# Performance work log

Hardware: AMD Instinct MI355X
Metric: run time of the kernel (lower is better)

Reference implementation:

```python
import jax, jax.numpy as jnp
import numpy as np

DIST_THRESH = 0.1
W_DIST = 0.05
W_CHAMFER = 0.05
W_SEP = 0.0005


def setup_inputs() -> dict:
    key = jax.random.key(0)
    k1, k2, k3, k4 = jax.random.split(key, 4)
    B, N, K = 4, 200000, 64
    return {
        "landmarks_C": jax.random.uniform(k1, (B, N, 3), jnp.float32),          # predicted point coords
        "landmarks_F": jax.random.normal(k2, (B, N, 4), jnp.float32) * 0.05,    # [dist, dx, dy, dz]
        "targets_C": jax.random.uniform(k3, (B, K, 3), jnp.float32),            # GT landmark coords
        "targets_F": jax.random.randint(k4, (B, K), 0, 8),                      # GT landmark class labels
        "classes": jnp.arange(6),                                               # classes to supervise
    }


def reference(landmarks_C, landmarks_F, targets_C, targets_F, classes):
    def per_batch(C_i, F_i, tC, tF):
        # class mask over GT landmarks (replaces boolean indexing in torch)
        mask_k = jnp.any(tF[None, :] == classes[:, None], axis=0)          # [K]
        n_valid = mask_k.sum()
        dists_i = F_i[:, 0]                                                # predicted distance, [N]
        coords_i = C_i + F_i[:, 1:]                                        # refined coords, [N,3]
        # pairwise dists GT landmarks -> raw point coords, invalid classes pushed to +inf
        pd = jnp.linalg.norm(C_i[None, :, :] - tC[:, None, :], axis=-1)    # [K,N]
        pd = jnp.where(mask_k[:, None], pd, jnp.inf)
        min_d = pd.min(axis=0)                                             # [N]
        pm = min_d < DIST_THRESH                                           # points near some GT landmark
        # smooth-L1 (beta=1, sum) on predicted distance; clip(inf)=2*thresh reproduces empty-target fallback
        tgt = jnp.clip(min_d, 0.0, 2.0 * DIST_THRESH)
        diff = dists_i - tgt
        ad = jnp.abs(diff)
        dist_loss = jnp.where(ad < 1.0, 0.5 * diff * diff, ad - 0.5).sum()
        # pairwise dists GT landmarks -> refined coords
        ld = jnp.linalg.norm(coords_i[None, :, :] - tC[:, None, :], axis=-1)  # [K,N]
        ld_m = jnp.where(mask_k[:, None], ld, jnp.inf)
        p2g = jnp.where(pm, ld_m.min(axis=0), 0.0)                         # pred->gt, masked points only
        g2p = jnp.where(mask_k, ld_m.min(axis=1), 0.0)                     # gt->pred, valid GT only
        chamfer = (p2g * p2g).sum() + (g2p * g2p).sum()
        # separation: ratio of dists to 2 nearest (valid) GT landmarks, per masked point
        _, idx = jax.lax.top_k(-pd.T, 2)                                   # [N,2] indices of 2 smallest
        d01 = jnp.take_along_axis(ld.T, idx, axis=1)                       # [N,2]
        sep = jnp.where(pm, d01[:, 0] / d01[:, 1], 0.0).sum()
        sep = jnp.where(n_valid >= 2, sep, 0.0)
        return W_DIST * dist_loss + W_CHAMFER * chamfer + W_SEP * sep

    losses = jax.vmap(per_batch)(landmarks_C, landmarks_F, targets_C, targets_F)
    return losses.mean()
```

## Files before the change

kernel.cpp:

```cpp
#include <hip/hip_runtime.h>


constexpr int KT = 64;
constexpr int P  = 8;
constexpr int NREP = 16;
constexpr float DIST_THRESH = 0.1f;
constexpr float W_DIST    = 0.05f;
constexpr float W_CHAMFER = 0.05f;
constexpr float W_SEP     = 0.0005f;
constexpr float PT_SENT = -1e18f;
constexpr float TG_SENT = -1e18f;
constexpr float BIGF  = 3.0e38f;
constexpr float WBIAS = 16.0f;

typedef float f2 __attribute__((ext_vector_type(2)));

__device__ __forceinline__ unsigned umin_(unsigned a, unsigned b) { return a < b ? a : b; }
__device__ __forceinline__ unsigned umax_(unsigned a, unsigned b) { return a > b ? a : b; }

__device__ __forceinline__ f2 pk_fma(f2 a, f2 b, f2 c) {
#if __has_builtin(__builtin_elementwise_fma)
    return __builtin_elementwise_fma(a, b, c);
#else
    f2 r; r.x = fmaf(a.x, b.x, c.x); r.y = fmaf(a.y, b.y, c.y); return r;
#endif
}

__global__ __launch_bounds__(128, 3)
void landmark_main(const float* __restrict__ C, const float* __restrict__ F,
                   const float* __restrict__ tC, const int* __restrict__ tF,
                   const int* __restrict__ classes, int n_classes,
                   int N, unsigned int* __restrict__ g2p_rep,
                   float* __restrict__ sums_rep)
{
    __shared__ float4 tgtH2[2][64];
    __shared__ float4 tgtFull[KT];
    __shared__ unsigned g2pLDS[KT];
    __shared__ unsigned mK1[64][P];
    __shared__ unsigned mK2[64][P];
    __shared__ float    mLM[64][P];

    const int tid   = threadIdx.x;
    const int lane  = tid & 63;
    const int h     = tid >> 6;
    const int l31   = lane & 31;
    const int blk   = blockIdx.x;
    const int b     = blk & 3;
    const int chunk = blk >> 2;
    const int rep   = chunk & (NREP - 1);
    const unsigned kbase = (unsigned)(h << 5);

    if (tid < KT) {
        int f = tF[b * KT + tid];
        bool valid = false;
        for (int c = 0; c < n_classes; ++c) valid = valid || (f == classes[c]);
        float x = TG_SENT, y = TG_SENT, z = TG_SENT;
        if (valid) {
            x = tC[(b * KT + tid) * 3 + 0];
            y = tC[(b * KT + tid) * 3 + 1];
            z = tC[(b * KT + tid) * 3 + 2];
        }
        float4 v = make_float4(-2.f * x, -2.f * y, -2.f * z,
                               x * x + y * y + z * z + WBIAS);
        tgtFull[tid] = v;
        int hh = tid >> 5, j = tid & 31;
        tgtH2[hh][j] = v;
        tgtH2[hh][j + 32] = v;
        g2pLDS[tid] = 0x7F7FFFFFu;
    }
    __syncthreads();

    const float*  Cb = C + (size_t)b * N * 3;
    const float4* Fb = (const float4*)(F + (size_t)b * N * 4);
    const int base = chunk * (64 * P);

    f2 pcx[P], pcy[P], pcz[P];
    float ccm[P], f0[P];
    #pragma unroll
    for (int p = 0; p < P; ++p) {
        int n = base + p * 64 + lane;
        bool v = (n < N);
        int ni = v ? n : 0;
        float4 f4 = Fb[ni];
        float X = Cb[3 * ni + 0], Y = Cb[3 * ni + 1], Z = Cb[3 * ni + 2];
        f0[p] = v ? f4.x : 2.0f * DIST_THRESH;
        if (!v) { X = PT_SENT; Y = PT_SENT; Z = PT_SENT; f4.y = f4.z = f4.w = 0.f; }
        float cxv = X + f4.y, cyv = Y + f4.z, czv = Z + f4.w;
        pcx[p] = (f2){X, cxv};
        pcy[p] = (f2){Y, cyv};
        pcz[p] = (f2){Z, czv};
        ccm[p] = fmaf(czv, czv, fmaf(cyv, cyv, cxv * cxv)) - WBIAS;
    }

    unsigned k1[P], k2[P];
    float lmin[P];
    #pragma unroll
    for (int p = 0; p < P; ++p) { k1[p] = 0xFFFFFFFFu; k2[p] = 0xFFFFFFFFu; lmin[p] = BIGF; }

    const float4* TH = tgtH2[h];

    #pragma unroll 4
    for (int i = 0; i < 32; ++i) {
        const float4 T = TH[l31 + i];
        const unsigned tk = kbase | (unsigned)((l31 + i) & 31);
        const f2 Tx = {T.x, T.x}, Ty = {T.y, T.y}, Tz = {T.z, T.z}, Tw = {T.w, T.w};
        float av[P];
        #pragma unroll
        for (int p = 0; p < P; ++p) {
            f2 w = pk_fma(pcx[p], Tx, pk_fma(pcy[p], Ty, pk_fma(pcz[p], Tz, Tw)));
            unsigned key = (__float_as_uint(w.x) & 0xFFFFFFC0u) | tk;
            unsigned hi = umax_(k1[p], key);
            k1[p] = umin_(k1[p], key);
            k2[p] = umin_(k2[p], hi);
            lmin[p] = fminf(lmin[p], w.y);
            av[p] = w.y + ccm[p];
        }
        float dl = fminf(fminf(fminf(av[0], av[1]), fminf(av[2], av[3])),
                         fminf(fminf(av[4], av[5]), fminf(av[6], av[7])));
        dl = fmaxf(dl, 0.f);
        atomicMin(&g2pLDS[tk], __float_as_uint(dl));
    }

    if (h == 0) {
        #pragma unroll
        for (int p = 0; p < P; ++p) {
            mK1[lane][p] = k1[p];
            mK2[lane][p] = k2[p];
            mLM[lane][p] = lmin[p];
        }
    }
    __syncthreads();

    if (h == 0) {
        atomicMax(&g2p_rep[rep * 256 + b * 64 + lane], ~g2pLDS[lane]);
    } else {
        float dist_acc = 0.f, p2g_acc = 0.f, sep_acc = 0.f;
        #pragma unroll
        for (int p = 0; p < P; ++p) {
            unsigned a1 = mK1[lane][p], a2 = mK2[lane][p];
            float    al = mLM[lane][p];
            unsigned m1 = umin_(a1, k1[p]);
            unsigned m2 = umin_(umax_(a1, k1[p]), umin_(a2, k2[p]));
            float lm = fminf(al, lmin[p]);
            float X = pcx[p].x, Y = pcy[p].x, Z = pcz[p].x;
            float ppm = fmaf(Z, Z, fmaf(Y, Y, X * X)) - WBIAS;
            float keyf1 = __uint_as_float(m1 & 0xFFFFFFC0u);
            float mind = sqrtf(fmaxf(keyf1 + ppm, 0.f));
            bool pm = mind < DIST_THRESH;
            float tgtv = fminf(mind, 2.0f * DIST_THRESH);
            float diff = f0[p] - tgtv;
            float ad = fabsf(diff);
            dist_acc += (ad < 1.0f) ? 0.5f * diff * diff : (ad - 0.5f);
            if (pm) {
                p2g_acc += fmaxf(lm + ccm[p], 0.f);
                int i1 = (int)(m1 & 63u), i2 = (int)(m2 & 63u);
                float4 T1 = tgtFull[i1], T2 = tgtFull[i2];
                float cxv = pcx[p].y, cyv = pcy[p].y, czv = pcz[p].y;
                float l1sq = fmaf(cxv, T1.x, fmaf(cyv, T1.y, fmaf(czv, T1.z, T1.w))) + ccm[p];
                float l2sq = fmaf(cxv, T2.x, fmaf(cyv, T2.y, fmaf(czv, T2.z, T2.w))) + ccm[p];
                sep_acc += sqrtf(fmaxf(l1sq, 0.f) / fmaxf(l2sq, 1e-30f));
            }
        }

        float v0 = dist_acc, v1 = p2g_acc, v2 = sep_acc;
        #pragma unroll
        for (int o = 32; o > 0; o >>= 1) {
            v0 += __shfl_down(v0, o, 64);
            v1 += __shfl_down(v1, o, 64);
            v2 += __shfl_down(v2, o, 64);
        }
        if (lane == 0) {
            float* sb = sums_rep + rep * 16 + b;
            atomicAdd(sb + 0, v0);
            atomicAdd(sb + 4, v1);
            atomicAdd(sb + 8, v2);
        }
    }
}

__global__ void landmark_finalize(const int* __restrict__ tF, const int* __restrict__ classes,
                                  int n_classes, const unsigned int* __restrict__ g2p_rep,
                                  const float* __restrict__ sums_rep, float* __restrict__ out)
{
    __shared__ float lossb[4];
    const int tid = threadIdx.x;
    const int b = tid >> 6, k = tid & 63;

    int f = tF[b * KT + k];
    bool valid = false;
    for (int c = 0; c < n_classes; ++c) valid = valid || (f == classes[c]);

    unsigned enc = 0;
    for (int r = 0; r < NREP; ++r) enc = umax_(enc, g2p_rep[r * 256 + b * 64 + k]);
    float g  = valid ? __uint_as_float(~enc) : 0.f;
    float nv = valid ? 1.f : 0.f;

    #pragma unroll
    for (int o = 32; o > 0; o >>= 1) {
        g  += __shfl_down(g, o, 64);
        nv += __shfl_down(nv, o, 64);
    }
    if (k == 0) {
        float sd = 0.f, sp = 0.f, ss = 0.f;
        for (int r = 0; r < NREP; ++r) {
            sd += sums_rep[r * 16 + 0 + b];
            sp += sums_rep[r * 16 + 4 + b];
            ss += sums_rep[r * 16 + 8 + b];
        }
        float sep = (nv >= 2.f) ? ss : 0.f;
        lossb[b] = W_DIST * sd + W_CHAMFER * (sp + g) + W_SEP * sep;
    }
    __syncthreads();
    if (tid == 0)
        out[0] = (lossb[0] + lossb[1] + lossb[2] + lossb[3]) * 0.25f;
}

extern "C" void kernel_launch(void* const* d_in, const int* in_sizes, int n_in,
                              void* d_out, int out_size, void* d_ws, size_t ws_size,
                              hipStream_t stream)
{
    const float* C       = (const float*)d_in[0];
    const float* F       = (const float*)d_in[1];
    const float* tC      = (const float*)d_in[2];
    const int*   tF      = (const int*)d_in[3];
    const int*   classes = (const int*)d_in[4];
    const int n_classes = in_sizes[4];
    const int B = 4;
    const int N = in_sizes[0] / (3 * B);

    unsigned int* g2p_rep  = (unsigned int*)d_ws;
    float*        sums_rep = (float*)((char*)d_ws + NREP * 256 * 4);

    hipMemsetAsync(d_ws, 0, NREP * 256 * 4 + NREP * 16 * 4, stream);

    const int cpb = (N + 64 * P - 1) / (64 * P);
    landmark_main<<<cpb * 4, 128, 0, stream>>>(C, F, tC, tF, classes, n_classes,
                                               N, g2p_rep, sums_rep);
    landmark_finalize<<<1, 256, 0, stream>>>(tF, classes, n_classes, g2p_rep,
                                             sums_rep, (float*)d_out);
}
```

Measured before the change: 103.7 us.

## Split targets across four waves, precompute targets in setup kernel, shuffle-reduce g2p

Target preprocessing (class masking, packed -2x/|x|^2 form) moves into a separate one-block setup kernel that writes to workspace. The main kernel now uses 256-thread blocks with 4 points per lane instead of 8, and each wave takes a 16-target slice. Each wave reads its targets as uniform (scalar) global loads instead of the rotated LDS copy. The per-target gt->pred minimum is reduced with cross-lane xor shuffles and one lane's global atomics, replacing per-iteration LDS atomicMin. Per-point top-2 keys from three waves are merged through LDS by the fourth wave. The aim is more parallelism and less LDS traffic, at the cost of an extra kernel launch and a sizeable shuffle reduction.

Result: slower. 172.0 us (+65.9%).

```diff
diff --git a/kernel.cpp b/kernel.cpp
--- a/kernel.cpp
+++ b/kernel.cpp
@@ -2,7 +2,7 @@
 
 
 constexpr int KT = 64;
-constexpr int P  = 8;
+constexpr int P  = 4;
 constexpr int NREP = 16;
 constexpr float DIST_THRESH = 0.1f;
 constexpr float W_DIST    = 0.05f;
@@ -26,49 +26,46 @@
 #endif
 }
 
-__global__ __launch_bounds__(128, 3)
+
+__global__ void landmark_setup(const float* __restrict__ tC, const int* __restrict__ tF,
+                               const int* __restrict__ classes, int n_classes,
+                               float4* __restrict__ tws)
+{
+    const int t = threadIdx.x;
+    const int b = t >> 6, k = t & 63;
+    int f = tF[b * KT + k];
+    bool valid = false;
+    for (int c = 0; c < n_classes; ++c) valid = valid || (f == classes[c]);
+    float x = TG_SENT, y = TG_SENT, z = TG_SENT;
+    if (valid) {
+        x = tC[(b * KT + k) * 3 + 0];
+        y = tC[(b * KT + k) * 3 + 1];
+        z = tC[(b * KT + k) * 3 + 2];
+    }
+    tws[b * KT + k] = make_float4(-2.f * x, -2.f * y, -2.f * z,
+                                  x * x + y * y + z * z + WBIAS);
+}
+
+__global__ __launch_bounds__(256, 4)
 void landmark_main(const float* __restrict__ C, const float* __restrict__ F,
-                   const float* __restrict__ tC, const int* __restrict__ tF,
-                   const int* __restrict__ classes, int n_classes,
-                   int N, unsigned int* __restrict__ g2p_rep,
-                   float* __restrict__ sums_rep)
-{
-    __shared__ float4 tgtH2[2][64];
-    __shared__ float4 tgtFull[KT];
-    __shared__ unsigned g2pLDS[KT];
-    __shared__ unsigned mK1[64][P];
-    __shared__ unsigned mK2[64][P];
-    __shared__ float    mLM[64][P];
+                   const float4* __restrict__ tws, int N,
+                   unsigned int* __restrict__ g2p_rep, float* __restrict__ sums_rep)
+{
+    __shared__ float4 tgtLDS[KT];
+    __shared__ uint4  pubK1[3][64];
+    __shared__ uint4  pubK2[3][64];
+    __shared__ float4 pubLM[3][64];
 
     const int tid   = threadIdx.x;
     const int lane  = tid & 63;
-    const int h     = tid >> 6;
-    const int l31   = lane & 31;
+    const int wib   = tid >> 6;
+    const int ksplit = __builtin_amdgcn_readfirstlane(wib);
     const int blk   = blockIdx.x;
     const int b     = blk & 3;
     const int chunk = blk >> 2;
     const int rep   = chunk & (NREP - 1);
-    const unsigned kbase = (unsigned)(h << 5);
-
-    if (tid < KT) {
-        int f = tF[b * KT + tid];
-        bool valid = false;
-        for (int c = 0; c < n_classes; ++c) valid = valid || (f == classes[c]);
-        float x = TG_SENT, y = TG_SENT, z = TG_SENT;
-        if (valid) {
-            x = tC[(b * KT + tid) * 3 + 0];
-            y = tC[(b * KT + tid) * 3 + 1];
-            z = tC[(b * KT + tid) * 3 + 2];
-        }
-        float4 v = make_float4(-2.f * x, -2.f * y, -2.f * z,
-                               x * x + y * y + z * z + WBIAS);
-        tgtFull[tid] = v;
-        int hh = tid >> 5, j = tid & 31;
-        tgtH2[hh][j] = v;
-        tgtH2[hh][j + 32] = v;
-        g2pLDS[tid] = 0x7F7FFFFFu;
-    }
-    __syncthreads();
+
+    if (wib == 0) tgtLDS[lane] = tws[b * KT + lane];
 
     const float*  Cb = C + (size_t)b * N * 3;
     const float4* Fb = (const float4*)(F + (size_t)b * N * 4);
@@ -93,16 +90,16 @@
     }
 
     unsigned k1[P], k2[P];
-    float lmin[P];
+    float lmin[P], dlreg[16];
     #pragma unroll
     for (int p = 0; p < P; ++p) { k1[p] = 0xFFFFFFFFu; k2[p] = 0xFFFFFFFFu; lmin[p] = BIGF; }
 
-    const float4* TH = tgtH2[h];
-
-    #pragma unroll 4
-    for (int i = 0; i < 32; ++i) {
-        const float4 T = TH[l31 + i];
-        const unsigned tk = kbase | (unsigned)((l31 + i) & 31);
+    const float4* tb = tws + b * KT + ksplit * 16;
+
+    #pragma unroll
+    for (int i = 0; i < 16; ++i) {
+        const float4 T = tb[i];
+        const unsigned tk = (unsigned)(ksplit * 16 + i);
         const f2 Tx = {T.x, T.x}, Ty = {T.y, T.y}, Tz = {T.z, T.z}, Tw = {T.w, T.w};
         float av[P];
         #pragma unroll
@@ -115,33 +112,49 @@
             lmin[p] = fminf(lmin[p], w.y);
             av[p] = w.y + ccm[p];
         }
-        float dl = fminf(fminf(fminf(av[0], av[1]), fminf(av[2], av[3])),
-                         fminf(fminf(av[4], av[5]), fminf(av[6], av[7])));
-        dl = fmaxf(dl, 0.f);
-        atomicMin(&g2pLDS[tk], __float_as_uint(dl));
-    }
-
-    if (h == 0) {
+        dlreg[i] = fmaxf(fminf(fminf(av[0], av[1]), fminf(av[2], av[3])), 0.f);
+    }
+
+    #pragma unroll
+    for (int d = 1; d < 64; d <<= 1) {
+        #pragma unroll
+        for (int i = 0; i < 16; ++i)
+            dlreg[i] = fminf(dlreg[i], __shfl_xor(dlreg[i], d, 64));
+    }
+    if (lane == 0) {
+        unsigned gb = rep * 256 + b * 64 + ksplit * 16;
+        #pragma unroll
+        for (int i = 0; i < 16; ++i)
+            atomicMax(&g2p_rep[gb + i], ~__float_as_uint(dlreg[i]));
+    }
+
+    if (wib < 3) {
+        pubK1[wib][lane] = make_uint4(k1[0], k1[1], k1[2], k1[3]);
+        pubK2[wib][lane] = make_uint4(k2[0], k2[1], k2[2], k2[3]);
+        pubLM[wib][lane] = make_float4(lmin[0], lmin[1], lmin[2], lmin[3]);
+    }
+    __syncthreads();
+
+    if (wib == 3) {
+        float dist_acc = 0.f, p2g_acc = 0.f, sep_acc = 0.f;
+        uint4 K1s[3], K2s[3]; float4 LMs[3];
+        #pragma unroll
+        for (int w = 0; w < 3; ++w) {
+            K1s[w] = pubK1[w][lane]; K2s[w] = pubK2[w][lane]; LMs[w] = pubLM[w][lane];
+        }
         #pragma unroll
         for (int p = 0; p < P; ++p) {
-            mK1[lane][p] = k1[p];
-            mK2[lane][p] = k2[p];
-            mLM[lane][p] = lmin[p];
-        }
-    }
-    __syncthreads();
-
-    if (h == 0) {
-        atomicMax(&g2p_rep[rep * 256 + b * 64 + lane], ~g2pLDS[lane]);
-    } else {
-        float dist_acc = 0.f, p2g_acc = 0.f, sep_acc = 0.f;
-        #pragma unroll
-        for (int p = 0; p < P; ++p) {
-            unsigned a1 = mK1[lane][p], a2 = mK2[lane][p];
-            float    al = mLM[lane][p];
-            unsigned m1 = umin_(a1, k1[p]);
-            unsigned m2 = umin_(umax_(a1, k1[p]), umin_(a2, k2[p]));
-            float lm = fminf(al, lmin[p]);
+            unsigned m1 = k1[p], m2 = k2[p];
+            float lm = lmin[p];
+            #pragma unroll
+            for (int w = 0; w < 3; ++w) {
+                unsigned o1 = (p == 0) ? K1s[w].x : (p == 1) ? K1s[w].y : (p == 2) ? K1s[w].z : K1s[w].w;
+                unsigned o2 = (p == 0) ? K2s[w].x : (p == 1) ? K2s[w].y : (p == 2) ? K2s[w].z : K2s[w].w;
+                float    ol = (p == 0) ? LMs[w].x : (p == 1) ? LMs[w].y : (p == 2) ? LMs[w].z : LMs[w].w;
+                m2 = umin_(umax_(m1, o1), umin_(m2, o2));
+                m1 = umin_(m1, o1);
+                lm = fminf(lm, ol);
+            }
             float X = pcx[p].x, Y = pcy[p].x, Z = pcz[p].x;
             float ppm = fmaf(Z, Z, fmaf(Y, Y, X * X)) - WBIAS;
             float keyf1 = __uint_as_float(m1 & 0xFFFFFFC0u);
@@ -154,7 +167,7 @@
             if (pm) {
                 p2g_acc += fmaxf(lm + ccm[p], 0.f);
                 int i1 = (int)(m1 & 63u), i2 = (int)(m2 & 63u);
-                float4 T1 = tgtFull[i1], T2 = tgtFull[i2];
+                float4 T1 = tgtLDS[i1], T2 = tgtLDS[i2];
                 float cxv = pcx[p].y, cyv = pcy[p].y, czv = pcz[p].y;
                 float l1sq = fmaf(cxv, T1.x, fmaf(cyv, T1.y, fmaf(czv, T1.z, T1.w))) + ccm[p];
                 float l2sq = fmaf(cxv, T2.x, fmaf(cyv, T2.y, fmaf(czv, T2.z, T2.w))) + ccm[p];
@@ -230,12 +243,14 @@
 
     unsigned int* g2p_rep  = (unsigned int*)d_ws;
     float*        sums_rep = (float*)((char*)d_ws + NREP * 256 * 4);
+    float4*       tws      = (float4*)((char*)d_ws + NREP * 256 * 4 + NREP * 16 * 4);
 
     hipMemsetAsync(d_ws, 0, NREP * 256 * 4 + NREP * 16 * 4, stream);
 
+    landmark_setup<<<1, 256, 0, stream>>>(tC, tF, classes, n_classes, tws);
+
     const int cpb = (N + 64 * P - 1) / (64 * P);
-    landmark_main<<<cpb * 4, 128, 0, stream>>>(C, F, tC, tF, classes, n_classes,
-                                               N, g2p_rep, sums_rep);
+    landmark_main<<<cpb * 4, 256, 0, stream>>>(C, F, tws, N, g2p_rep, sums_rep);
     landmark_finalize<<<1, 256, 0, stream>>>(tF, classes, n_classes, g2p_rep,
                                              sums_rep, (float*)d_out);
 }
```

## Split target halves within a wave and merge top-2 via cross-half shuffles

Applied to the files above, without the earlier changes.

Each wave now handles its own chunk of points: the two 32-lane halves each scan 32 targets over 4 points per lane (an XOR-indexed target walk instead of a duplicated target table), and the per-point top-2 keys and min values are merged with a lane-xor-32 shuffle instead of a shared-memory exchange between two waves. Blocks grow to 256 threads holding four independent waves, with one block-level reduction of the partial sums before the global atomics. The aim is to drop the block-wide sync and LDS round trip of the old two-wave split and to lower per-thread register load for better occupancy. In exchange there are more shuffles, fewer points per thread to amortize each target fetch, and a 4-way reduction step.

After: 105.4 us. Within noise of the previous version (+1.7%).

```diff
diff --git a/kernel.cpp b/kernel.cpp
--- a/kernel.cpp
+++ b/kernel.cpp
@@ -2,7 +2,7 @@
 
 
 constexpr int KT = 64;
-constexpr int P  = 8;
+constexpr int P  = 4;
 constexpr int NREP = 16;
 constexpr float DIST_THRESH = 0.1f;
 constexpr float W_DIST    = 0.05f;
@@ -26,29 +26,26 @@
 #endif
 }
 
-__global__ __launch_bounds__(128, 3)
+__global__ __launch_bounds__(256, 6)
 void landmark_main(const float* __restrict__ C, const float* __restrict__ F,
                    const float* __restrict__ tC, const int* __restrict__ tF,
                    const int* __restrict__ classes, int n_classes,
-                   int N, unsigned int* __restrict__ g2p_rep,
-                   float* __restrict__ sums_rep)
+                   int N, int cpb,
+                   unsigned int* __restrict__ g2p_rep, float* __restrict__ sums_rep)
 {
-    __shared__ float4 tgtH2[2][64];
-    __shared__ float4 tgtFull[KT];
+    __shared__ float4 tgt[KT];
     __shared__ unsigned g2pLDS[KT];
-    __shared__ unsigned mK1[64][P];
-    __shared__ unsigned mK2[64][P];
-    __shared__ float    mLM[64][P];
+    __shared__ float rs[3][4];
 
     const int tid   = threadIdx.x;
     const int lane  = tid & 63;
-    const int h     = tid >> 6;
+    const int wib   = tid >> 6;
     const int l31   = lane & 31;
+    const int half  = lane >> 5;
     const int blk   = blockIdx.x;
     const int b     = blk & 3;
-    const int chunk = blk >> 2;
-    const int rep   = chunk & (NREP - 1);
-    const unsigned kbase = (unsigned)(h << 5);
+    const int chunk = (blk >> 2) * 4 + wib;
+    const int rep   = blk & (NREP - 1);
 
     if (tid < KT) {
         int f = tF[b * KT + tid];
@@ -60,91 +57,78 @@
             y = tC[(b * KT + tid) * 3 + 1];
             z = tC[(b * KT + tid) * 3 + 2];
         }
-        float4 v = make_float4(-2.f * x, -2.f * y, -2.f * z,
+        tgt[tid] = make_float4(-2.f * x, -2.f * y, -2.f * z,
                                x * x + y * y + z * z + WBIAS);
-        tgtFull[tid] = v;
-        int hh = tid >> 5, j = tid & 31;
-        tgtH2[hh][j] = v;
-        tgtH2[hh][j + 32] = v;
         g2pLDS[tid] = 0x7F7FFFFFu;
     }
     __syncthreads();
 
-    const float*  Cb = C + (size_t)b * N * 3;
-    const float4* Fb = (const float4*)(F + (size_t)b * N * 4);
-    const int base = chunk * (64 * P);
-
-    f2 pcx[P], pcy[P], pcz[P];
-    float ccm[P], f0[P];
-    #pragma unroll
-    for (int p = 0; p < P; ++p) {
-        int n = base + p * 64 + lane;
-        bool v = (n < N);
-        int ni = v ? n : 0;
-        float4 f4 = Fb[ni];
-        float X = Cb[3 * ni + 0], Y = Cb[3 * ni + 1], Z = Cb[3 * ni + 2];
-        f0[p] = v ? f4.x : 2.0f * DIST_THRESH;
-        if (!v) { X = PT_SENT; Y = PT_SENT; Z = PT_SENT; f4.y = f4.z = f4.w = 0.f; }
-        float cxv = X + f4.y, cyv = Y + f4.z, czv = Z + f4.w;
-        pcx[p] = (f2){X, cxv};
-        pcy[p] = (f2){Y, cyv};
-        pcz[p] = (f2){Z, czv};
-        ccm[p] = fmaf(czv, czv, fmaf(cyv, cyv, cxv * cxv)) - WBIAS;
-    }
-
-    unsigned k1[P], k2[P];
-    float lmin[P];
-    #pragma unroll
-    for (int p = 0; p < P; ++p) { k1[p] = 0xFFFFFFFFu; k2[p] = 0xFFFFFFFFu; lmin[p] = BIGF; }
-
-    const float4* TH = tgtH2[h];
-
-    #pragma unroll 4
-    for (int i = 0; i < 32; ++i) {
-        const float4 T = TH[l31 + i];
-        const unsigned tk = kbase | (unsigned)((l31 + i) & 31);
-        const f2 Tx = {T.x, T.x}, Ty = {T.y, T.y}, Tz = {T.z, T.z}, Tw = {T.w, T.w};
-        float av[P];
+    float dist_acc = 0.f, p2g_acc = 0.f, sep_acc = 0.f;
+
+    if (chunk < cpb) {
+        const float*  Cb = C + (size_t)b * N * 3;
+        const float4* Fb = (const float4*)(F + (size_t)b * N * 4);
+        const int base = chunk * (32 * P);
+
+        f2 pcx[P], pcy[P], pcz[P];
+        float ccm[P], f0[P];
         #pragma unroll
         for (int p = 0; p < P; ++p) {
-            f2 w = pk_fma(pcx[p], Tx, pk_fma(pcy[p], Ty, pk_fma(pcz[p], Tz, Tw)));
-            unsigned key = (__float_as_uint(w.x) & 0xFFFFFFC0u) | tk;
-            unsigned hi = umax_(k1[p], key);
-            k1[p] = umin_(k1[p], key);
-            k2[p] = umin_(k2[p], hi);
-            lmin[p] = fminf(lmin[p], w.y);
-            av[p] = w.y + ccm[p];
-        }
-        float dl = fminf(fminf(fminf(av[0], av[1]), fminf(av[2], av[3])),
-                         fminf(fminf(av[4], av[5]), fminf(av[6], av[7])));
-        dl = fmaxf(dl, 0.f);
-        atomicMin(&g2pLDS[tk], __float_as_uint(dl));
-    }
-
-    if (h == 0) {
+            int n = base + p * 32 + l31;
+            bool v = (n < N);
+            int ni = v ? n : 0;
+            float4 f4 = Fb[ni];
+            float X = Cb[3 * ni + 0], Y = Cb[3 * ni + 1], Z = Cb[3 * ni + 2];
+            f0[p] = v ? f4.x : 2.0f * DIST_THRESH;
+            if (!v) { X = PT_SENT; Y = PT_SENT; Z = PT_SENT; f4.y = f4.z = f4.w = 0.f; }
+            float cxv = X + f4.y, cyv = Y + f4.z, czv = Z + f4.w;
+            pcx[p] = (f2){X, cxv};
+            pcy[p] = (f2){Y, cyv};
+            pcz[p] = (f2){Z, czv};
+            ccm[p] = fmaf(czv, czv, fmaf(cyv, cyv, cxv * cxv)) - WBIAS;
+        }
+
+        unsigned k1[P], k2[P];
+        float lmin[P];
+        #pragma unroll
+        for (int p = 0; p < P; ++p) { k1[p] = 0xFFFFFFFFu; k2[p] = 0xFFFFFFFFu; lmin[p] = BIGF; }
+
+        #pragma unroll 8
+        for (int i = 0; i < 32; ++i) {
+            const unsigned tk = (unsigned)(lane ^ i);
+            const float4 T = tgt[tk];
+            const f2 Tx = {T.x, T.x}, Ty = {T.y, T.y}, Tz = {T.z, T.z}, Tw = {T.w, T.w};
+            float av[P];
+            #pragma unroll
+            for (int p = 0; p < P; ++p) {
+                f2 w = pk_fma(pcx[p], Tx, pk_fma(pcy[p], Ty, pk_fma(pcz[p], Tz, Tw)));
+                unsigned key = (__float_as_uint(w.x) & 0xFFFFFFC0u) | tk;
+                unsigned hi = umax_(k1[p], key);
+                k1[p] = umin_(k1[p], key);
+                k2[p] = umin_(k2[p], hi);
+                lmin[p] = fminf(lmin[p], w.y);
+                av[p] = w.y + ccm[p];
+            }
+            float dl = fmaxf(fminf(fminf(av[0], av[1]), fminf(av[2], av[3])), 0.f);
+            atomicMin(&g2pLDS[tk], __float_as_uint(dl));
+        }
+
         #pragma unroll
         for (int p = 0; p < P; ++p) {
-            mK1[lane][p] = k1[p];
-            mK2[lane][p] = k2[p];
-            mLM[lane][p] = lmin[p];
-        }
-    }
-    __syncthreads();
-
-    if (h == 0) {
-        atomicMax(&g2p_rep[rep * 256 + b * 64 + lane], ~g2pLDS[lane]);
-    } else {
-        float dist_acc = 0.f, p2g_acc = 0.f, sep_acc = 0.f;
-        #pragma unroll
-        for (int p = 0; p < P; ++p) {
-            unsigned a1 = mK1[lane][p], a2 = mK2[lane][p];
-            float    al = mLM[lane][p];
-            unsigned m1 = umin_(a1, k1[p]);
-            unsigned m2 = umin_(umax_(a1, k1[p]), umin_(a2, k2[p]));
-            float lm = fminf(al, lmin[p]);
+            unsigned o1 = (unsigned)__shfl_xor((int)k1[p], 32, 64);
+            unsigned o2 = (unsigned)__shfl_xor((int)k2[p], 32, 64);
+            k2[p] = umin_(umax_(k1[p], o1), umin_(k2[p], o2));
+            k1[p] = umin_(k1[p], o1);
+            lmin[p] = fminf(lmin[p], __shfl_xor(lmin[p], 32, 64));
+        }
+
+        const int p0 = half * (P / 2);
+        #pragma unroll
+        for (int pp = 0; pp < P / 2; ++pp) {
+            const int p = p0 + pp;
             float X = pcx[p].x, Y = pcy[p].x, Z = pcz[p].x;
             float ppm = fmaf(Z, Z, fmaf(Y, Y, X * X)) - WBIAS;
-            float keyf1 = __uint_as_float(m1 & 0xFFFFFFC0u);
+            float keyf1 = __uint_as_float(k1[p] & 0xFFFFFFC0u);
             float mind = sqrtf(fmaxf(keyf1 + ppm, 0.f));
             bool pm = mind < DIST_THRESH;
             float tgtv = fminf(mind, 2.0f * DIST_THRESH);
@@ -152,29 +136,33 @@
             float ad = fabsf(diff);
             dist_acc += (ad < 1.0f) ? 0.5f * diff * diff : (ad - 0.5f);
             if (pm) {
-                p2g_acc += fmaxf(lm + ccm[p], 0.f);
-                int i1 = (int)(m1 & 63u), i2 = (int)(m2 & 63u);
-                float4 T1 = tgtFull[i1], T2 = tgtFull[i2];
+                p2g_acc += fmaxf(lmin[p] + ccm[p], 0.f);
+                int i1 = (int)(k1[p] & 63u), i2 = (int)(k2[p] & 63u);
+                float4 T1 = tgt[i1], T2 = tgt[i2];
                 float cxv = pcx[p].y, cyv = pcy[p].y, czv = pcz[p].y;
                 float l1sq = fmaf(cxv, T1.x, fmaf(cyv, T1.y, fmaf(czv, T1.z, T1.w))) + ccm[p];
                 float l2sq = fmaf(cxv, T2.x, fmaf(cyv, T2.y, fmaf(czv, T2.z, T2.w))) + ccm[p];
                 sep_acc += sqrtf(fmaxf(l1sq, 0.f) / fmaxf(l2sq, 1e-30f));
             }
         }
-
-        float v0 = dist_acc, v1 = p2g_acc, v2 = sep_acc;
-        #pragma unroll
-        for (int o = 32; o > 0; o >>= 1) {
-            v0 += __shfl_down(v0, o, 64);
-            v1 += __shfl_down(v1, o, 64);
-            v2 += __shfl_down(v2, o, 64);
-        }
-        if (lane == 0) {
-            float* sb = sums_rep + rep * 16 + b;
-            atomicAdd(sb + 0, v0);
-            atomicAdd(sb + 4, v1);
-            atomicAdd(sb + 8, v2);
-        }
+    }
+
+    float v0 = dist_acc, v1 = p2g_acc, v2 = sep_acc;
+    #pragma unroll
+    for (int o = 32; o > 0; o >>= 1) {
+        v0 += __shfl_down(v0, o, 64);
+        v1 += __shfl_down(v1, o, 64);
+        v2 += __shfl_down(v2, o, 64);
+    }
+    if (lane == 0) { rs[0][wib] = v0; rs[1][wib] = v1; rs[2][wib] = v2; }
+    __syncthreads();
+
+    if (tid < KT) {
+        atomicMax(&g2p_rep[rep * 256 + b * 64 + tid], ~g2pLDS[tid]);
+    }
+    if (tid < 3) {
+        float s = rs[tid][0] + rs[tid][1] + rs[tid][2] + rs[tid][3];
+        atomicAdd(&sums_rep[rep * 16 + tid * 4 + b], s);
     }
 }
 
@@ -233,9 +221,10 @@
 
     hipMemsetAsync(d_ws, 0, NREP * 256 * 4 + NREP * 16 * 4, stream);
 
-    const int cpb = (N + 64 * P - 1) / (64 * P);
-    landmark_main<<<cpb * 4, 128, 0, stream>>>(C, F, tC, tF, classes, n_classes,
-                                               N, g2p_rep, sums_rep);
+    const int cpb = (N + 32 * P - 1) / (32 * P);
+    const int bpb = (cpb + 3) / 4;
+    landmark_main<<<bpb * 4, 256, 0, stream>>>(C, F, tC, tF, classes, n_classes,
+                                               N, cpb, g2p_rep, sums_rep);
     landmark_finalize<<<1, 256, 0, stream>>>(tF, classes, n_classes, g2p_rep,
                                              sums_rep, (float*)d_out);
 }
```
